# Kernel tuning notes

Hardware: AMD Instinct MI355X
Metric: run time of the kernel (lower is better)

Reference implementation:

```python
import jax, jax.numpy as jnp
import numpy as np


def setup_inputs() -> dict:
    key = jax.random.key(0)
    k1, k2, k3, k4 = jax.random.split(key, 4)
    H, D, Dh, NH = 4096, 1024, 256, 4  # height, weight1, INNER_FEATURE_A, heads
    x = jax.random.normal(k1, (H, D), dtype=jnp.float32)
    Wq = jax.random.normal(k2, (NH, D, Dh), dtype=jnp.float32)
    lin_w = jax.random.normal(k3, (D, NH * Dh), dtype=jnp.float32)  # torch Linear weight [out, in]
    lin_b = jax.random.normal(k4, (D,), dtype=jnp.float32)
    return {"x": x, "Wq": Wq, "lin_w": lin_w, "lin_b": lin_b}


def reference(x, Wq, lin_w, lin_b):
    # Faithful to source: Q = K = V = x @ Wq1 (original uses Wq1 for all three).
    # mask_flag=False -> multiplicative all-ones mask (identity, elided).
    # qkv: [heads, H, Dh]
    qkv = jnp.einsum('hd,ndk->nhk', x, Wq)
    # scores: [heads, H, H]; softmax over dim=1 of the 2D matrix = last axis here
    scores = jnp.einsum('nqk,npk->nqp', qkv, qkv)
    attn = jax.nn.softmax(scores, axis=-1)
    z = jnp.einsum('nqp,npk->nqk', attn, qkv)  # [heads, H, Dh]
    # concat heads along feature dim -> [H, heads*Dh]
    zc = jnp.transpose(z, (1, 0, 2)).reshape(x.shape[0], -1)
    return zc @ lin_w.T + lin_b
```

## Files before the change

### kernel.cpp

```cpp
#include <hip/hip_runtime.h>
#include <math.h>

#define SEQ 4096
#define DIM 1024
#define DHEAD 256
#define NHEADS 4

typedef __attribute__((ext_vector_type(8))) short bf16x8;
typedef __attribute__((ext_vector_type(4))) float f32x4;
typedef __attribute__((ext_vector_type(4))) short short4v;
typedef __attribute__((ext_vector_type(8))) short short8v;

__device__ __forceinline__ unsigned short f2b(float f) {
    union { float f; unsigned u; } v; v.f = f;
    unsigned r = v.u + 0x7FFFu + ((v.u >> 16) & 1u);
    return (unsigned short)(r >> 16);
}
__device__ __forceinline__ float b2f(unsigned short u) {
    union { unsigned u; float f; } v; v.u = ((unsigned)u) << 16;
    return v.f;
}

__device__ __forceinline__ void gll16(const void* g, void* lds) {
    __builtin_amdgcn_global_load_lds(
        (const __attribute__((address_space(1))) unsigned*)g,
        (__attribute__((address_space(3))) unsigned*)lds, 16, 0, 0);
}

__device__ __forceinline__ f32x4 mfma16(bf16x8 a, bf16x8 b, f32x4 c) {
    return __builtin_amdgcn_mfma_f32_16x16x32_bf16(a, b, c, 0, 0, 0);
}

__global__ __launch_bounds__(256)
void conv_kernel(const float* __restrict__ in, unsigned short* __restrict__ out, int n4) {
    int i = blockIdx.x * 256 + threadIdx.x;
    if (i >= n4) return;
    float4 v = ((const float4*)in)[i];
    short4v o;
    o[0] = (short)f2b(v.x); o[1] = (short)f2b(v.y);
    o[2] = (short)f2b(v.z); o[3] = (short)f2b(v.w);
    *(short4v*)(out + (size_t)i * 4) = o;
}

__global__ __launch_bounds__(256)
void wqt_kernel(const float* __restrict__ Wq, unsigned short* __restrict__ WqT) {
    __shared__ unsigned short T[64][72];
    const int tid = threadIdx.x;
    const int h = blockIdx.z;
    const int d0 = blockIdx.x * 64, c0 = blockIdx.y * 64;
#pragma unroll
    for (int it = 0; it < 4; ++it) {
        int f = tid + 256 * it;
        int row = f >> 4, cg = f & 15;
        float4 v = *(const float4*)&Wq[((size_t)(h * DIM + d0 + row)) * DHEAD + c0 + cg * 4];
        T[row][cg * 4 + 0] = f2b(v.x); T[row][cg * 4 + 1] = f2b(v.y);
        T[row][cg * 4 + 2] = f2b(v.z); T[row][cg * 4 + 3] = f2b(v.w);
    }
    __syncthreads();
#pragma unroll
    for (int it = 0; it < 2; ++it) {
        int f = tid + 256 * it;
        int cl = f >> 3, dg = f & 7;
        short8v o;
#pragma unroll
        for (int e = 0; e < 8; ++e) o[e] = (short)T[dg * 8 + e][cl];
        *(short8v*)&WqT[((size_t)(h * DHEAD + c0 + cl)) * DIM + d0 + dg * 8] = o;
    }
}

__global__ __launch_bounds__(256)
void qkv_gemm_kernel(const unsigned short* __restrict__ A,
                     const unsigned short* __restrict__ B,
                     unsigned short* __restrict__ qkv,
                     unsigned short* __restrict__ qkvT) {
    __shared__ unsigned short As[128 * 64];
    __shared__ unsigned short Bs[128 * 64];
    const int tid = threadIdx.x, w = tid >> 6, l = tid & 63;
    const int g = l >> 4, r16 = l & 15;
    const int m0 = blockIdx.x * 128, n0 = blockIdx.y * 128;
    const int wm = (w >> 1) * 64, wn = (w & 1) * 64;

    f32x4 acc[4][4];
#pragma unroll
    for (int mr = 0; mr < 4; ++mr)
#pragma unroll
        for (int nr = 0; nr < 4; ++nr) acc[mr][nr] = (f32x4){0.f, 0.f, 0.f, 0.f};

    for (int kb = 0; kb < DIM; kb += 64) {
        __syncthreads();
#pragma unroll
        for (int cc = 0; cc < 4; ++cc) {
            int row = w * 32 + cc * 8 + (l >> 3);
            int c = (l & 7) ^ (row & 7);
            gll16(&A[(size_t)(m0 + row) * DIM + kb + c * 8], &As[(size_t)(w * 32 + cc * 8) * 64]);
            gll16(&B[(size_t)(n0 + row) * DIM + kb + c * 8], &Bs[(size_t)(w * 32 + cc * 8) * 64]);
        }
        __syncthreads();
#pragma unroll
        for (int s = 0; s < 2; ++s) {
            bf16x8 af[4], bf[4];
#pragma unroll
            for (int mr = 0; mr < 4; ++mr) {
                int row = wm + mr * 16 + r16;
                int st = (s * 4 + g) ^ (row & 7);
                af[mr] = *(const bf16x8*)&As[row * 64 + st * 8];
            }
#pragma unroll
            for (int nr = 0; nr < 4; ++nr) {
                int row = wn + nr * 16 + r16;
                int st = (s * 4 + g) ^ (row & 7);
                bf[nr] = *(const bf16x8*)&Bs[row * 64 + st * 8];
            }
#pragma unroll
            for (int mr = 0; mr < 4; ++mr)
#pragma unroll
                for (int nr = 0; nr < 4; ++nr)
                    acc[mr][nr] = mfma16(af[mr], bf[nr], acc[mr][nr]);
        }
    }
#pragma unroll
    for (int mr = 0; mr < 4; ++mr)
#pragma unroll
        for (int nr = 0; nr < 4; ++nr) {
            int n = n0 + wn + nr * 16 + r16;
            int h = n >> 8, c = n & 255;
            int mb = m0 + wm + mr * 16 + g * 4;
            short4v tv;
#pragma unroll
            for (int r = 0; r < 4; ++r) {
                unsigned short b = f2b(acc[mr][nr][r]);
                qkv[((size_t)h * SEQ + mb + r) * DHEAD + c] = b;
                tv[r] = (short)b;
            }
            *(short4v*)&qkvT[((size_t)h * DHEAD + c) * SEQ + mb] = tv;
        }
}

__global__ __launch_bounds__(256, 2)
void attn_kernel(const unsigned short* __restrict__ qkv,
                 const unsigned short* __restrict__ qkvT,
                 unsigned short* __restrict__ p0,
                 unsigned short* __restrict__ p1,
                 float* __restrict__ ml) {
    __shared__ unsigned short Ks[2][64 * 256];
    __shared__ unsigned short Ps[64 * 64];
    __shared__ float alphaS[64];
    __shared__ float mS[64], lS[64];

    const int tid = threadIdx.x, w = tid >> 6, l = tid & 63;
    const int g = l >> 4, r16 = l & 15;
    const int bid = blockIdx.x;
    const int h = (bid & 7) >> 1, hf = bid & 1;
    const int qb = bid >> 3;
    const unsigned short* __restrict__ qh = qkv + (size_t)h * SEQ * DHEAD;
    const unsigned short* __restrict__ qth = qkvT + (size_t)h * DHEAD * SEQ;
    const int jb0 = hf * (SEQ / 2);
    const int NT = (SEQ / 2) / 64;

    bf16x8 qf[8];
    {
        const unsigned short* qrow = qh + (size_t)(qb * 64 + w * 16 + r16) * DHEAD + g * 8;
#pragma unroll
        for (int s = 0; s < 8; ++s) qf[s] = *(const bf16x8*)(qrow + s * 32);
    }

#define STAGEK(buf, jb)                                                             \
    {                                                                               \
        _Pragma("unroll")                                                           \
        for (int cc = 0; cc < 8; ++cc) {                                            \
            int ch = w * 8 + cc;                                                    \
            int j = ch * 2 + (l >> 5);                                              \
            int cp = l & 31;                                                        \
            int c = (cp & 24) | ((cp & 7) ^ (j & 7));                               \
            gll16(&qh[(size_t)((jb) + j) * DHEAD + c * 8], &Ks[buf][(size_t)ch * 512]); \
        }                                                                           \
    }

    STAGEK(0, jb0);

    f32x4 Oacc[16];
#pragma unroll
    for (int i = 0; i < 16; ++i) Oacc[i] = (f32x4){0.f, 0.f, 0.f, 0.f};
    float mrow = -INFINITY, lrow = 0.f;

    for (int t = 0; t < NT; ++t) {
        const int cur = t & 1;
        const int jb = jb0 + t * 64;

        __builtin_amdgcn_sched_barrier(0);
        asm volatile("s_waitcnt vmcnt(0)" ::: "memory");
        __builtin_amdgcn_s_barrier();
        __builtin_amdgcn_sched_barrier(0);

        bf16x8 bv[4][2];
#pragma unroll
        for (int dt = 0; dt < 4; ++dt) {
            int d = w * 64 + dt * 16 + r16;
#pragma unroll
            for (int s2 = 0; s2 < 2; ++s2)
                bv[dt][s2] = *(const bf16x8*)&qth[(size_t)d * SEQ + jb + s2 * 32 + g * 8];
        }
        __builtin_amdgcn_sched_barrier(0);

        if (t + 1 < NT) STAGEK(cur ^ 1, jb0 + (t + 1) * 64);
        __builtin_amdgcn_sched_barrier(0);

        const unsigned short* Kb = &Ks[cur][0];
        f32x4 sacc[4];
#pragma unroll
        for (int jt = 0; jt < 4; ++jt) sacc[jt] = (f32x4){0.f, 0.f, 0.f, 0.f};
        __builtin_amdgcn_s_setprio(1);
#pragma unroll
        for (int s = 0; s < 8; ++s)
#pragma unroll
            for (int jt = 0; jt < 4; ++jt) {
                int j = jt * 16 + r16;
                int c = s * 4 + g;
                int st = (c & 24) | ((c & 7) ^ (j & 7));
                bf16x8 af = *(const bf16x8*)&Kb[j * 256 + st * 8];
                sacc[jt] = mfma16(af, qf[s], sacc[jt]);
            }
        __builtin_amdgcn_s_setprio(0);

        float mx = sacc[0][0];
#pragma unroll
        for (int jt = 0; jt < 4; ++jt)
#pragma unroll
            for (int r = 0; r < 4; ++r) mx = fmaxf(mx, sacc[jt][r]);
        mx = fmaxf(mx, __shfl_xor(mx, 16, 64));
        mx = fmaxf(mx, __shfl_xor(mx, 32, 64));

        float alpha = 1.f;
        if (!__all(mx <= mrow + 8.f)) {
            float mn = fmaxf(mrow, mx);
            alpha = __expf(mrow - mn);
            mrow = mn;
        }

        float rsum = 0.f;
        short4v pf[4];
#pragma unroll
        for (int jt = 0; jt < 4; ++jt)
#pragma unroll
            for (int r = 0; r < 4; ++r) {
                float p = __expf(sacc[jt][r] - mrow);
                rsum += p;
                pf[jt][r] = (short)f2b(p);
            }
        rsum += __shfl_xor(rsum, 16, 64);
        rsum += __shfl_xor(rsum, 32, 64);
        lrow = lrow * alpha + rsum;

#pragma unroll
        for (int jt = 0; jt < 4; ++jt) {
            int st = (jt * 2 + (g >> 1)) ^ (r16 & 7);
            *(short4v*)&Ps[(w * 16 + r16) * 64 + st * 8 + (g & 1) * 4] = pf[jt];
        }
        if (g == 0) alphaS[w * 16 + r16] = alpha;

        __builtin_amdgcn_sched_barrier(0);
        asm volatile("s_waitcnt lgkmcnt(0)" ::: "memory");
        __builtin_amdgcn_s_barrier();
        __builtin_amdgcn_sched_barrier(0);

        bf16x8 pa[8];
#pragma unroll
        for (int qs = 0; qs < 4; ++qs) {
            f32x4 av = *(const f32x4*)&alphaS[qs * 16 + g * 4];
            if (!__all((av[0] == 1.f) & (av[1] == 1.f) & (av[2] == 1.f) & (av[3] == 1.f))) {
#pragma unroll
                for (int dt = 0; dt < 4; ++dt)
#pragma unroll
                    for (int r = 0; r < 4; ++r) Oacc[qs * 4 + dt][r] *= av[r];
            }
#pragma unroll
            for (int s2 = 0; s2 < 2; ++s2) {
                int qrow = qs * 16 + r16;
                int st = (s2 * 4 + g) ^ (qrow & 7);
                pa[qs * 2 + s2] = *(const bf16x8*)&Ps[qrow * 64 + st * 8];
            }
        }
        __builtin_amdgcn_s_setprio(1);
#pragma unroll
        for (int dt = 0; dt < 4; ++dt)
#pragma unroll
            for (int s2 = 0; s2 < 2; ++s2)
#pragma unroll
                for (int qs = 0; qs < 4; ++qs)
                    Oacc[qs * 4 + dt] = mfma16(pa[qs * 2 + s2], bv[dt][s2], Oacc[qs * 4 + dt]);
        __builtin_amdgcn_s_setprio(0);
    }
#undef STAGEK

    asm volatile("s_waitcnt vmcnt(0)" ::: "memory");

    if (g == 0) { mS[w * 16 + r16] = mrow; lS[w * 16 + r16] = lrow; }
    __syncthreads();
    unsigned short* po = hf ? p1 : p0;
#pragma unroll
    for (int qs = 0; qs < 4; ++qs)
#pragma unroll
        for (int dt = 0; dt < 4; ++dt) {
            int d = w * 64 + dt * 16 + r16;
#pragma unroll
            for (int r = 0; r < 4; ++r) {
                int q = qb * 64 + qs * 16 + g * 4 + r;
                po[(size_t)q * (NHEADS * DHEAD) + h * DHEAD + d] = f2b(Oacc[qs * 4 + dt][r]);
            }
        }
    if (tid < 64) {
        int q = qb * 64 + tid;
        float* mlq = ml + ((size_t)(hf * NHEADS + h) * SEQ + q) * 2;
        mlq[0] = mS[tid]; mlq[1] = lS[tid];
    }
}

__global__ __launch_bounds__(256)
void combine_kernel(const unsigned short* __restrict__ pa,
                    const unsigned short* __restrict__ pb,
                    const float* __restrict__ ml,
                    unsigned short* __restrict__ zc) {
    size_t t = (size_t)blockIdx.x * 256 + threadIdx.x;
    size_t f = t * 8;
    int q = (int)(f >> 10);
    int h = (int)((f >> 8) & 3);
    const float* ml0 = ml + ((size_t)h * SEQ + q) * 2;
    const float* ml1 = ml + ((size_t)(NHEADS + h) * SEQ + q) * 2;
    float m0 = ml0[0], l0 = ml0[1], m1 = ml1[0], l1 = ml1[1];
    float M = fmaxf(m0, m1);
    float e0 = __expf(m0 - M), e1 = __expf(m1 - M);
    float inv = 1.f / (e0 * l0 + e1 * l1);
    e0 *= inv; e1 *= inv;
    short8v a = *(const short8v*)(pa + f);
    short8v b = *(const short8v*)(pb + f);
    short8v o;
#pragma unroll
    for (int e = 0; e < 8; ++e)
        o[e] = (short)f2b(e0 * b2f((unsigned short)a[e]) + e1 * b2f((unsigned short)b[e]));
    *(short8v*)(zc + f) = o;
}

__global__ __launch_bounds__(256)
void out_gemm_kernel(const unsigned short* __restrict__ A,
                     const unsigned short* __restrict__ B,
                     const float* __restrict__ lb, float* __restrict__ out) {
    __shared__ unsigned short As[128 * 64];
    __shared__ unsigned short Bs[128 * 64];
    const int tid = threadIdx.x, w = tid >> 6, l = tid & 63;
    const int g = l >> 4, r16 = l & 15;
    const int m0 = blockIdx.x * 128, n0 = blockIdx.y * 128;
    const int wm = (w >> 1) * 64, wn = (w & 1) * 64;

    f32x4 acc[4][4];
#pragma unroll
    for (int mr = 0; mr < 4; ++mr)
#pragma unroll
        for (int nr = 0; nr < 4; ++nr) acc[mr][nr] = (f32x4){0.f, 0.f, 0.f, 0.f};

    for (int kb = 0; kb < DIM; kb += 64) {
        __syncthreads();
#pragma unroll
        for (int cc = 0; cc < 4; ++cc) {
            int row = w * 32 + cc * 8 + (l >> 3);
            int c = (l & 7) ^ (row & 7);
            gll16(&A[(size_t)(m0 + row) * DIM + kb + c * 8], &As[(size_t)(w * 32 + cc * 8) * 64]);
            gll16(&B[(size_t)(n0 + row) * DIM + kb + c * 8], &Bs[(size_t)(w * 32 + cc * 8) * 64]);
        }
        __syncthreads();
#pragma unroll
        for (int s = 0; s < 2; ++s) {
            bf16x8 af[4], bf[4];
#pragma unroll
            for (int mr = 0; mr < 4; ++mr) {
                int row = wm + mr * 16 + r16;
                int st = (s * 4 + g) ^ (row & 7);
                af[mr] = *(const bf16x8*)&As[row * 64 + st * 8];
            }
#pragma unroll
            for (int nr = 0; nr < 4; ++nr) {
                int row = wn + nr * 16 + r16;
                int st = (s * 4 + g) ^ (row & 7);
                bf[nr] = *(const bf16x8*)&Bs[row * 64 + st * 8];
            }
#pragma unroll
            for (int mr = 0; mr < 4; ++mr)
#pragma unroll
                for (int nr = 0; nr < 4; ++nr)
                    acc[mr][nr] = mfma16(af[mr], bf[nr], acc[mr][nr]);
        }
    }
#pragma unroll
    for (int mr = 0; mr < 4; ++mr)
#pragma unroll
        for (int nr = 0; nr < 4; ++nr) {
            int n = n0 + wn + nr * 16 + r16;
            float bv = lb[n];
#pragma unroll
            for (int r = 0; r < 4; ++r) {
                int m = m0 + wm + mr * 16 + g * 4 + r;
                out[(size_t)m * DIM + n] = acc[mr][nr][r] + bv;
            }
        }
}

extern "C" void kernel_launch(void* const* d_in, const int* in_sizes, int n_in,
                              void* d_out, int out_size, void* d_ws, size_t ws_size,
                              hipStream_t stream) {
    const float* x  = (const float*)d_in[0];
    const float* Wq = (const float*)d_in[1];
    const float* lw = (const float*)d_in[2];
    const float* lb = (const float*)d_in[3];
    float* out = (float*)d_out;

    char* wsb = (char*)d_ws;
    unsigned short* qkvb = (unsigned short*)(wsb);
    unsigned short* qkvT = (unsigned short*)(wsb + ((size_t)8 << 20));
    unsigned short* xb   = (unsigned short*)(wsb + ((size_t)16 << 20));
    unsigned short* p0   = xb;
    unsigned short* WqT  = (unsigned short*)(wsb + ((size_t)24 << 20));
    float*          ml   = (float*)(wsb + ((size_t)24 << 20));
    unsigned short* lwb  = (unsigned short*)(wsb + ((size_t)26 << 20));
    unsigned short* p1   = (unsigned short*)d_out;

    conv_kernel<<<4096, 256, 0, stream>>>(x, xb, (SEQ * DIM) / 4);
    conv_kernel<<<1024, 256, 0, stream>>>(lw, lwb, (DIM * DIM) / 4);
    wqt_kernel<<<dim3(16, 4, 4), 256, 0, stream>>>(Wq, WqT);
    qkv_gemm_kernel<<<dim3(SEQ / 128, DIM / 128), 256, 0, stream>>>(xb, WqT, qkvb, qkvT);
    attn_kernel<<<512, 256, 0, stream>>>(qkvb, qkvT, p0, p1, ml);
    combine_kernel<<<(SEQ * DIM / 8) / 256, 256, 0, stream>>>(p0, p1, ml, p0);
    out_gemm_kernel<<<dim3(SEQ / 128, DIM / 128), 256, 0, stream>>>(p0, lwb, lb, out);
}
```

Measured before the change: 179.9 us.

## Stage V tiles through LDS with 32-key tiles and separate transpose kernel

The attention kernel's key tile shrinks from 64 to 32. V (the transposed qkv) is now staged into LDS with async global-to-LDS loads, replacing direct per-wave global register loads, and each step waits on it with a partial vmcnt. The scattered transposed writes in the QKV GEMM epilogue move into a separate LDS-tiled transpose kernel. This should cut LDS usage and improve occupancy and global access coalescing, at the cost of twice as many loop iterations with their barriers and an extra kernel launch plus a full re-read of qkv.

```diff
diff --git a/kernel.cpp b/kernel.cpp
--- a/kernel.cpp
+++ b/kernel.cpp
@@ -69,10 +69,35 @@
 }
 
 __global__ __launch_bounds__(256)
+void qkvt_kernel(const unsigned short* __restrict__ qkv, unsigned short* __restrict__ qkvT) {
+    __shared__ unsigned short T[64][72];
+    const int tid = threadIdx.x;
+    const int h = blockIdx.z;
+    const int r0 = blockIdx.x * 64, c0 = blockIdx.y * 64;
+#pragma unroll
+    for (int it = 0; it < 2; ++it) {
+        int f = tid + 256 * it;
+        int row = f >> 3, cg = f & 7;
+        short8v v = *(const short8v*)&qkv[((size_t)h * SEQ + r0 + row) * DHEAD + c0 + cg * 8];
+#pragma unroll
+        for (int e = 0; e < 8; ++e) T[row][cg * 8 + e] = (unsigned short)v[e];
+    }
+    __syncthreads();
+#pragma unroll
+    for (int it = 0; it < 2; ++it) {
+        int f = tid + 256 * it;
+        int cl = f >> 3, rg = f & 7;
+        short8v o;
+#pragma unroll
+        for (int e = 0; e < 8; ++e) o[e] = (short)T[rg * 8 + e][cl];
+        *(short8v*)&qkvT[((size_t)h * DHEAD + c0 + cl) * SEQ + r0 + rg * 8] = o;
+    }
+}
+
+__global__ __launch_bounds__(256)
 void qkv_gemm_kernel(const unsigned short* __restrict__ A,
                      const unsigned short* __restrict__ B,
-                     unsigned short* __restrict__ qkv,
-                     unsigned short* __restrict__ qkvT) {
+                     unsigned short* __restrict__ qkv) {
     __shared__ unsigned short As[128 * 64];
     __shared__ unsigned short Bs[128 * 64];
     const int tid = threadIdx.x, w = tid >> 6, l = tid & 63;
@@ -124,15 +149,11 @@
         for (int nr = 0; nr < 4; ++nr) {
             int n = n0 + wn + nr * 16 + r16;
             int h = n >> 8, c = n & 255;
-            int mb = m0 + wm + mr * 16 + g * 4;
-            short4v tv;
 #pragma unroll
             for (int r = 0; r < 4; ++r) {
-                unsigned short b = f2b(acc[mr][nr][r]);
-                qkv[((size_t)h * SEQ + mb + r) * DHEAD + c] = b;
-                tv[r] = (short)b;
-            }
-            *(short4v*)&qkvT[((size_t)h * DHEAD + c) * SEQ + mb] = tv;
+                int m = m0 + wm + mr * 16 + g * 4 + r;
+                qkv[((size_t)h * SEQ + m) * DHEAD + c] = f2b(acc[mr][nr][r]);
+            }
         }
 }
 
@@ -142,8 +163,9 @@
                  unsigned short* __restrict__ p0,
                  unsigned short* __restrict__ p1,
                  float* __restrict__ ml) {
-    __shared__ unsigned short Ks[2][64 * 256];
-    __shared__ unsigned short Ps[64 * 64];
+    __shared__ unsigned short Ks[2][32 * 256];
+    __shared__ unsigned short Vt[256 * 32];
+    __shared__ unsigned short Ps[64 * 32];
     __shared__ float alphaS[64];
     __shared__ float mS[64], lS[64];
 
@@ -155,7 +177,7 @@
     const unsigned short* __restrict__ qh = qkv + (size_t)h * SEQ * DHEAD;
     const unsigned short* __restrict__ qth = qkvT + (size_t)h * DHEAD * SEQ;
     const int jb0 = hf * (SEQ / 2);
-    const int NT = (SEQ / 2) / 64;
+    const int NT = (SEQ / 2) / 32;
 
     bf16x8 qf[8];
     {
@@ -167,14 +189,24 @@
 #define STAGEK(buf, jb)                                                             \
     {                                                                               \
         _Pragma("unroll")                                                           \
-        for (int cc = 0; cc < 8; ++cc) {                                            \
-            int ch = w * 8 + cc;                                                    \
+        for (int cc = 0; cc < 4; ++cc) {                                            \
+            int ch = w * 4 + cc;                          \
             int j = ch * 2 + (l >> 5);                                              \
             int cp = l & 31;                                                        \
             int c = (cp & 24) | ((cp & 7) ^ (j & 7));                               \
             gll16(&qh[(size_t)((jb) + j) * DHEAD + c * 8], &Ks[buf][(size_t)ch * 512]); \
         }                                                                           \
     }
+#define STAGEV(jb)                                                                  \
+    {                                                                               \
+        _Pragma("unroll")                                                           \
+        for (int cc = 0; cc < 4; ++cc) {                                            \
+            int ch = w * 4 + cc;                        \
+            int d = ch * 16 + (l >> 2);                                             \
+            int c = (l & 3) ^ (d & 3);                                              \
+            gll16(&qth[(size_t)d * SEQ + (jb) + c * 8], &Vt[(size_t)ch * 512]);     \
+        }                                                                           \
+    }
 
     STAGEK(0, jb0);
 
@@ -185,35 +217,27 @@
 
     for (int t = 0; t < NT; ++t) {
         const int cur = t & 1;
-        const int jb = jb0 + t * 64;
+        const int jb = jb0 + t * 32;
+        const int jbn = jb0 + ((t + 1) & (NT - 1)) * 32;
 
         __builtin_amdgcn_sched_barrier(0);
         asm volatile("s_waitcnt vmcnt(0)" ::: "memory");
         __builtin_amdgcn_s_barrier();
         __builtin_amdgcn_sched_barrier(0);
 
-        bf16x8 bv[4][2];
-#pragma unroll
-        for (int dt = 0; dt < 4; ++dt) {
-            int d = w * 64 + dt * 16 + r16;
-#pragma unroll
-            for (int s2 = 0; s2 < 2; ++s2)
-                bv[dt][s2] = *(const bf16x8*)&qth[(size_t)d * SEQ + jb + s2 * 32 + g * 8];
-        }
+        STAGEV(jb);
+        STAGEK(cur ^ 1, jbn);
         __builtin_amdgcn_sched_barrier(0);
 
-        if (t + 1 < NT) STAGEK(cur ^ 1, jb0 + (t + 1) * 64);
-        __builtin_amdgcn_sched_barrier(0);
-
         const unsigned short* Kb = &Ks[cur][0];
-        f32x4 sacc[4];
-#pragma unroll
-        for (int jt = 0; jt < 4; ++jt) sacc[jt] = (f32x4){0.f, 0.f, 0.f, 0.f};
+        f32x4 sacc[2];
+#pragma unroll
+        for (int jt = 0; jt < 2; ++jt) sacc[jt] = (f32x4){0.f, 0.f, 0.f, 0.f};
         __builtin_amdgcn_s_setprio(1);
 #pragma unroll
         for (int s = 0; s < 8; ++s)
 #pragma unroll
-            for (int jt = 0; jt < 4; ++jt) {
+            for (int jt = 0; jt < 2; ++jt) {
                 int j = jt * 16 + r16;
                 int c = s * 4 + g;
                 int st = (c & 24) | ((c & 7) ^ (j & 7));
@@ -224,7 +248,7 @@
 
         float mx = sacc[0][0];
 #pragma unroll
-        for (int jt = 0; jt < 4; ++jt)
+        for (int jt = 0; jt < 2; ++jt)
 #pragma unroll
             for (int r = 0; r < 4; ++r) mx = fmaxf(mx, sacc[jt][r]);
         mx = fmaxf(mx, __shfl_xor(mx, 16, 64));
@@ -238,9 +262,9 @@
         }
 
         float rsum = 0.f;
-        short4v pf[4];
-#pragma unroll
-        for (int jt = 0; jt < 4; ++jt)
+        short4v pf[2];
+#pragma unroll
+        for (int jt = 0; jt < 2; ++jt)
 #pragma unroll
             for (int r = 0; r < 4; ++r) {
                 float p = __expf(sacc[jt][r] - mrow);
@@ -252,20 +276,23 @@
         lrow = lrow * alpha + rsum;
 
 #pragma unroll
-        for (int jt = 0; jt < 4; ++jt) {
-            int st = (jt * 2 + (g >> 1)) ^ (r16 & 7);
-            *(short4v*)&Ps[(w * 16 + r16) * 64 + st * 8 + (g & 1) * 4] = pf[jt];
+        for (int jt = 0; jt < 2; ++jt) {
+            int st = (2 * jt + (g >> 1)) ^ ((r16 >> 2) & 3);
+            *(short4v*)&Ps[(w * 16 + r16) * 32 + st * 8 + (g & 1) * 4] = pf[jt];
         }
         if (g == 0) alphaS[w * 16 + r16] = alpha;
 
         __builtin_amdgcn_sched_barrier(0);
-        asm volatile("s_waitcnt lgkmcnt(0)" ::: "memory");
+        asm volatile("s_waitcnt vmcnt(4) lgkmcnt(0)" ::: "memory");
         __builtin_amdgcn_s_barrier();
         __builtin_amdgcn_sched_barrier(0);
 
-        bf16x8 pa[8];
+        bf16x8 pa[4];
 #pragma unroll
         for (int qs = 0; qs < 4; ++qs) {
+            int q = qs * 16 + r16;
+            int st = g ^ ((q >> 2) & 3);
+            pa[qs] = *(const bf16x8*)&Ps[q * 32 + st * 8];
             f32x4 av = *(const f32x4*)&alphaS[qs * 16 + g * 4];
             if (!__all((av[0] == 1.f) & (av[1] == 1.f) & (av[2] == 1.f) & (av[3] == 1.f))) {
 #pragma unroll
@@ -273,24 +300,24 @@
 #pragma unroll
                     for (int r = 0; r < 4; ++r) Oacc[qs * 4 + dt][r] *= av[r];
             }
-#pragma unroll
-            for (int s2 = 0; s2 < 2; ++s2) {
-                int qrow = qs * 16 + r16;
-                int st = (s2 * 4 + g) ^ (qrow & 7);
-                pa[qs * 2 + s2] = *(const bf16x8*)&Ps[qrow * 64 + st * 8];
-            }
+        }
+        bf16x8 bv[4];
+#pragma unroll
+        for (int dt = 0; dt < 4; ++dt) {
+            int d = w * 64 + dt * 16 + r16;
+            int st = g ^ (d & 3);
+            bv[dt] = *(const bf16x8*)&Vt[d * 32 + st * 8];
         }
         __builtin_amdgcn_s_setprio(1);
 #pragma unroll
         for (int dt = 0; dt < 4; ++dt)
 #pragma unroll
-            for (int s2 = 0; s2 < 2; ++s2)
-#pragma unroll
-                for (int qs = 0; qs < 4; ++qs)
-                    Oacc[qs * 4 + dt] = mfma16(pa[qs * 2 + s2], bv[dt][s2], Oacc[qs * 4 + dt]);
+            for (int qs = 0; qs < 4; ++qs)
+                Oacc[qs * 4 + dt] = mfma16(pa[qs], bv[dt], Oacc[qs * 4 + dt]);
         __builtin_amdgcn_s_setprio(0);
     }
 #undef STAGEK
+#undef STAGEV
 
     asm volatile("s_waitcnt vmcnt(0)" ::: "memory");
 
@@ -425,7 +452,8 @@
     conv_kernel<<<4096, 256, 0, stream>>>(x, xb, (SEQ * DIM) / 4);
     conv_kernel<<<1024, 256, 0, stream>>>(lw, lwb, (DIM * DIM) / 4);
     wqt_kernel<<<dim3(16, 4, 4), 256, 0, stream>>>(Wq, WqT);
-    qkv_gemm_kernel<<<dim3(SEQ / 128, DIM / 128), 256, 0, stream>>>(xb, WqT, qkvb, qkvT);
+    qkv_gemm_kernel<<<dim3(SEQ / 128, DIM / 128), 256, 0, stream>>>(xb, WqT, qkvb);
+    qkvt_kernel<<<dim3(64, 4, 4), 256, 0, stream>>>(qkvb, qkvT);
     attn_kernel<<<512, 256, 0, stream>>>(qkvb, qkvT, p0, p1, ml);
     combine_kernel<<<(SEQ * DIM / 8) / 256, 256, 0, stream>>>(p0, p1, ml, p0);
     out_gemm_kernel<<<dim3(SEQ / 128, DIM / 128), 256, 0, stream>>>(p0, lwb, lb, out);
```

Result: slower. 195.2 us (+8.5%).
